# Performance work log

Measured on AMD Instinct MI355X. Metric: run time of the kernel, lower is better.

## Reference

```python
import jax, jax.numpy as jnp
import numpy as np

D = 768
CTX = 64


def ln(x, g, b, eps=1e-5):
    m = x.mean(-1, keepdims=True)
    v = jnp.mean((x - m) ** 2, -1, keepdims=True)
    return (x - m) / jnp.sqrt(v + eps) * g + b


def setup_inputs() -> dict:
    key = jax.random.key(0)
    ks = jax.random.split(key, 16)
    B, N = 16, 1024
    w = lambda k, shape: jax.random.normal(k, shape, dtype=jnp.float32) * 0.02
    return {
        'comps': jax.random.normal(ks[0], (8, B, N, D), jnp.float32),
        'geometric_context': jax.random.normal(ks[1], (B, N, D), jnp.float32),
        'question_features': jax.random.normal(ks[2], (B, D), jnp.float32),
        'spatial_mask': jax.random.randint(ks[3], (B,), 0, 2) > 0,
        'gp_w1': w(ks[4], (D, D // 2)), 'gp_b1': jnp.zeros((D // 2,)),
        'gp_g1': jnp.ones((D // 2,)), 'gp_be1': jnp.zeros((D // 2,)),
        'gp_w2': w(ks[5], (D // 2, CTX)), 'gp_b2': jnp.zeros((CTX,)),
        'swp_w1': w(ks[6], (CTX + D, 256)), 'swp_b1': jnp.zeros((256,)),
        'swp_g1': jnp.ones((256,)), 'swp_be1': jnp.zeros((256,)),
        'swp_w2': w(ks[7], (256, 128)), 'swp_b2': jnp.zeros((128,)),
        'swp_g2': jnp.ones((128,)), 'swp_be2': jnp.zeros((128,)),
        'swp_w3': w(ks[8], (128, 8)), 'swp_b3': jnp.zeros((8,)),
        'sw1': w(ks[9], (4, D + CTX, D)), 'sb1': jnp.zeros((4, D)),
        'sg1': jnp.ones((4, D)), 'sbe1': jnp.zeros((4, D)),
        'sw2': w(ks[10], (4, D, D)), 'sb2': jnp.zeros((4, D)),
        'sg2': jnp.ones((4, D)), 'sbe2': jnp.zeros((4, D)),
        'rw1': w(ks[11], (4, D + CTX, D)), 'rb1': jnp.zeros((4, D)),
        'rg1': jnp.ones((4, D)), 'rbe1': jnp.zeros((4, D)),
        'rw2': w(ks[12], (4, D, D)), 'rb2': jnp.zeros((4, D)),
    }


def reference(comps, geometric_context, question_features, spatial_mask,
              gp_w1, gp_b1, gp_g1, gp_be1, gp_w2, gp_b2,
              swp_w1, swp_b1, swp_g1, swp_be1, swp_w2, swp_b2, swp_g2, swp_be2, swp_w3, swp_b3,
              sw1, sb1, sg1, sbe1, sw2, sb2, sg2, sbe2,
              rw1, rb1, rg1, rbe1, rw2, rb2):
    B, N = geometric_context.shape[:2]
    # geometric_processor on mean-pooled context -> [B, 64]
    gcc = jax.nn.relu(ln(geometric_context.mean(1) @ gp_w1 + gp_b1, gp_g1, gp_be1)) @ gp_w2 + gp_b2
    # spatial_weight_predictor -> softmax weights [B, 8]
    wi = jnp.concatenate([gcc, question_features], -1)
    h = jax.nn.gelu(ln(wi @ swp_w1 + swp_b1, swp_g1, swp_be1), approximate=False)
    h = jax.nn.gelu(ln(h @ swp_w2 + swp_b2, swp_g2, swp_be2), approximate=False)
    aw = jax.nn.softmax(h @ swp_w3 + swp_b3, -1)
    # expanded context; non-spatial samples use 0.1-scaled context for spatial-set comps
    ctx = jnp.broadcast_to(gcc[:, None, :], (B, N, CTX))
    ctx_s = ctx * jnp.where(spatial_mask, 1.0, 0.1)[:, None, None]
    # strong enhancers (GELU, second LN): P_unique(0), V_unique(1), PV(3), PT(5) - all spatial-set
    xs = jnp.concatenate([comps[jnp.array([0, 1, 3, 5])],
                          jnp.broadcast_to(ctx_s, (4, B, N, CTX))], -1)
    h = jax.nn.gelu(ln(jnp.einsum('kbnd,kdf->kbnf', xs, sw1) + sb1[:, None, None, :],
                       sg1[:, None, None, :], sbe1[:, None, None, :]), approximate=False)
    ys = ln(jnp.einsum('kbnd,kdf->kbnf', h, sw2) + sb2[:, None, None, :],
            sg2[:, None, None, :], sbe2[:, None, None, :])
    # ReLU enhancers (moderate/minimal share structure): TV(4, scaled ctx), T_unique(2), redundant(6), higher(7)
    ctx_r = jnp.stack([ctx_s, ctx, ctx, ctx], 0)
    xr = jnp.concatenate([comps[jnp.array([4, 2, 6, 7])], ctx_r], -1)
    h = jax.nn.relu(ln(jnp.einsum('kbnd,kdf->kbnf', xr, rw1) + rb1[:, None, None, :],
                       rg1[:, None, None, :], rbe1[:, None, None, :]))
    yr = jnp.einsum('kbnd,kdf->kbnf', h, rw2) + rb2[:, None, None, :]
    # non-spatial components pass through when spatial_mask is False
    m = spatial_mask[:, None, None]
    out = jnp.stack([
        ys[0],                              # P_unique
        ys[1],                              # V_unique
        jnp.where(m, yr[1], comps[2]),      # T_unique
        ys[2],                              # PV_synergy
        yr[0],                              # TV_synergy
        ys[3],                              # PT_synergy
        jnp.where(m, yr[2], comps[6]),      # redundant
        jnp.where(m, yr[3], comps[7]),      # higher_synergy
    ], 0)
    return out, aw
```

## Files before the change

kernel.cpp:

```cpp
#include <hip/hip_runtime.h>
#include <math.h>

#define MT 16384
#define DD 768
#define AW_OFF ((size_t)8 * MT * DD)

typedef __attribute__((ext_vector_type(8))) short short8;
typedef __attribute__((ext_vector_type(4))) float f32x4;
typedef __attribute__((ext_vector_type(4))) float fv4;
typedef __attribute__((ext_vector_type(4))) unsigned int u32x4;

#define OFF_W1T 0ULL
#define OFF_W2T 10223616ULL
#define OFF_Z1  19660800ULL
#define OFF_Z2  220987392ULL
#define OFF_P1  321675264ULL
#define OFF_P2  324820992ULL
#define OFF_ST1 326393856ULL
#define OFF_ST2 327442432ULL
#define OFF_GP  327966720ULL
#define OFF_GM  328359936ULL
#define OFF_CXS 328409088ULL
#define OFF_CXU 328411136ULL
#define OFF_A1  335544320ULL

static __device__ __forceinline__ unsigned short f2bf(float f) {
  unsigned u = __float_as_uint(f);
  u += 0x7fffu + ((u >> 16) & 1u);
  return (unsigned short)(u >> 16);
}
static __device__ __forceinline__ float bf2f(unsigned short h) {
  return __uint_as_float(((unsigned)h) << 16);
}
static __device__ __forceinline__ unsigned pk2(float lo, float hi) {
  return (unsigned)f2bf(lo) | ((unsigned)f2bf(hi) << 16);
}
static __device__ __forceinline__ float gelu_t(float y) {
  float y2 = y * y;
  float c = fmaf(y2, 0.0713548163f, 1.59576912161f);
  float e = __expf(-y * c);
  return y / (1.0f + e);
}
static __device__ __forceinline__ void gload_lds16(const void* g, void* l) {
  __builtin_amdgcn_global_load_lds(
      (const __attribute__((address_space(1))) void*)g,
      (__attribute__((address_space(3))) void*)l, 16, 0, 0);
}

__global__ void transpose_cvt(const float* sw1, const float* rw1,
                              const float* sw2, const float* rw2,
                              unsigned short* w1T, unsigned short* w2T) {
  __shared__ float t[32][33];
  const int z = blockIdx.z;
  int R; const float* sp; unsigned short* dp;
  if (z < 8) {
    R = 832;
    sp = ((z < 4) ? sw1 : rw1) + (size_t)(z & 3) * 832 * DD;
    dp = w1T + (size_t)z * DD * 832;
  } else {
    R = 768;
    int zz = z - 8;
    sp = ((zz < 4) ? sw2 : rw2) + (size_t)(zz & 3) * DD * DD;
    dp = w2T + (size_t)zz * DD * DD;
  }
  const int r0 = blockIdx.x * 32, c0 = blockIdx.y * 32;
  if (r0 >= R) return;
  const int tx = threadIdx.x & 31, ty = threadIdx.x >> 5;
#pragma unroll
  for (int i = 0; i < 4; i++) {
    int r = ty + i * 8;
    t[r][tx] = sp[(size_t)(r0 + r) * DD + c0 + tx];
  }
  __syncthreads();
#pragma unroll
  for (int i = 0; i < 4; i++) {
    int cc = ty + i * 8;
    dp[(size_t)(c0 + cc) * R + r0 + tx] = f2bf(t[tx][cc]);
  }
}

__global__ void colmean1(const float* __restrict__ geo, float* __restrict__ gp) {
  const int b = blockIdx.z, yc = blockIdx.y;
  const int col = blockIdx.x * 256 + threadIdx.x;
  const float* p = geo + (size_t)b * 1024 * DD + (size_t)yc * 128 * DD + col;
  float s = 0.f;
  for (int n = 0; n < 128; ++n) s += p[(size_t)n * DD];
  gp[((size_t)b * 8 + yc) * DD + col] = s;
}
__global__ void colmean2(const float* __restrict__ gp, float* __restrict__ gm) {
  const int b = blockIdx.y;
  const int col = blockIdx.x * 256 + threadIdx.x;
  float s = 0.f;
#pragma unroll
  for (int i = 0; i < 8; ++i) s += gp[((size_t)b * 8 + i) * DD + col];
  gm[(size_t)b * DD + col] = s * (1.0f / 1024.0f);
}

static __device__ float2 blk_sum2(float a, float b, float* red) {
  const int tid = threadIdx.x;
  __syncthreads();
  red[tid] = a; red[512 + tid] = b;
  if (tid < 128) { red[384 + tid] = 0.f; red[512 + 384 + tid] = 0.f; }
  __syncthreads();
  for (int s = 256; s > 0; s >>= 1) {
    if (tid < s) { red[tid] += red[tid + s]; red[512 + tid] += red[512 + tid + s]; }
    __syncthreads();
  }
  return make_float2(red[0], red[512]);
}

__global__ void small_mlp(
    const float* __restrict__ gc_mean, const float* __restrict__ qf,
    const int* __restrict__ mask,
    const float* __restrict__ gp_w1, const float* __restrict__ gp_b1,
    const float* __restrict__ gp_g1, const float* __restrict__ gp_be1,
    const float* __restrict__ gp_w2, const float* __restrict__ gp_b2,
    const float* __restrict__ swp_w1, const float* __restrict__ swp_b1,
    const float* __restrict__ swp_g1, const float* __restrict__ swp_be1,
    const float* __restrict__ swp_w2, const float* __restrict__ swp_b2,
    const float* __restrict__ swp_g2, const float* __restrict__ swp_be2,
    const float* __restrict__ swp_w3, const float* __restrict__ swp_b3,
    unsigned short* __restrict__ ctxs, unsigned short* __restrict__ ctxu,
    float* __restrict__ aw)
{
  __shared__ float gm[768];
  __shared__ float buf[832];
  __shared__ float tmp[384];
  __shared__ float red[1024];
  const int b = blockIdx.x, tid = threadIdx.x;

  for (int i = tid; i < 768; i += 384) gm[i] = gc_mean[b * 768 + i];
  __syncthreads();

  float z = gp_b1[tid];
  for (int k = 0; k < 768; k++) z += gm[k] * gp_w1[k * 384 + tid];
  float2 s = blk_sum2(z, z * z, red);
  {
    float mean = s.x * (1.f / 384.f);
    float rinv = rsqrtf(s.y * (1.f / 384.f) - mean * mean + 1e-5f);
    float y = (z - mean) * rinv * gp_g1[tid] + gp_be1[tid];
    tmp[tid] = fmaxf(y, 0.f);
  }
  __syncthreads();

  if (tid < 64) {
    float g = gp_b2[tid];
    for (int k = 0; k < 384; k++) g += tmp[k] * gp_w2[k * 64 + tid];
    float sc = (mask[b] != 0) ? 1.0f : 0.1f;
    ctxs[b * 64 + tid] = f2bf(g * sc);
    ctxu[b * 64 + tid] = f2bf(g);
    buf[tid] = g;
  }
  for (int i = tid; i < 768; i += 384) buf[64 + i] = qf[b * 768 + i];
  __syncthreads();

  float z1 = 0.f;
  if (tid < 256) {
    z1 = swp_b1[tid];
    for (int k = 0; k < 832; k++) z1 += buf[k] * swp_w1[k * 256 + tid];
  }
  s = blk_sum2(z1, z1 * z1, red);
  {
    float mean = s.x * (1.f / 256.f);
    float rinv = rsqrtf(s.y * (1.f / 256.f) - mean * mean + 1e-5f);
    if (tid < 256) {
      float y = (z1 - mean) * rinv * swp_g1[tid] + swp_be1[tid];
      tmp[tid] = 0.5f * y * (1.f + erff(y * 0.7071067811865476f));
    }
  }
  __syncthreads();

  float z2 = 0.f;
  if (tid < 128) {
    z2 = swp_b2[tid];
    for (int k = 0; k < 256; k++) z2 += tmp[k] * swp_w2[k * 128 + tid];
  }
  s = blk_sum2(z2, z2 * z2, red);
  {
    float mean = s.x * (1.f / 128.f);
    float rinv = rsqrtf(s.y * (1.f / 128.f) - mean * mean + 1e-5f);
    if (tid < 128) {
      float y = (z2 - mean) * rinv * swp_g2[tid] + swp_be2[tid];
      tmp[tid] = 0.5f * y * (1.f + erff(y * 0.7071067811865476f));
    }
  }
  __syncthreads();

  if (tid < 8) {
    float z3 = swp_b3[tid];
    for (int k = 0; k < 128; k++) z3 += tmp[k] * swp_w3[k * 8 + tid];
    buf[tid] = z3;
  }
  __syncthreads();
  if (tid < 8) {
    float mx = buf[0];
    for (int k = 1; k < 8; k++) mx = fmaxf(mx, buf[k]);
    float ssum = 0.f;
    for (int k = 0; k < 8; k++) ssum += expf(buf[k] - mx);
    aw[b * 8 + tid] = expf(buf[tid] - mx) / ssum;
  }
}

__global__ void stats_k(const float2* __restrict__ part, float2* __restrict__ st,
                        int nr) {
  int i = blockIdx.x * 256 + threadIdx.x;
  if (i >= nr) return;
  float2 p0 = part[i], p1 = part[nr + i], p2 = part[2 * nr + i];
  float s1 = p0.x + p1.x + p2.x, s2 = p0.y + p1.y + p2.y;
  float mean = s1 * (1.f / 768.f);
  float var = s2 * (1.f / 768.f) - mean * mean;
  float rinv = rsqrtf(var + 1e-5f);
  st[i] = make_float2(rinv, -mean * rinv);
}

__global__ __launch_bounds__(512, 4)
void gemm1_k(const float* __restrict__ comps,
             const unsigned short* __restrict__ cxs,
             const unsigned short* __restrict__ cxu,
             const unsigned short* __restrict__ w1T,
             const float* __restrict__ sb1, const float* __restrict__ rb1,
             unsigned short* __restrict__ z1,
             float2* __restrict__ part1,
             const int* __restrict__ mask)
{
  __shared__ __align__(16) unsigned short As[2][4096];
  __shared__ __align__(16) unsigned short Bs[2][8192];
  __shared__ float pscr[4][128][2];
  constexpr int NT = 26;

  const int id = blockIdx.x;
  const int x = id & 7, j = id >> 3;
  const int br_nt = j >> 4;
  const int mt = ((j & 15) << 3) | x;
  const int nt = br_nt % 3;
  const int br = br_nt / 3;
  const int m0 = mt * 128, n0 = nt * 256;
  const int b = m0 >> 10;
  if (br >= 5 && mask[b] == 0) return;

  const int ci = (0x76245310u >> (br * 4)) & 15;
  const float* afp = comps + (size_t)ci * MT * DD + (size_t)m0 * DD;
  const unsigned short* ctxp = ((br <= 4) ? cxs : cxu) + b * 64;
  const unsigned short* wT = w1T + (size_t)br * DD * 832 + (size_t)n0 * 832;

  const int tid = threadIdx.x;
  const int w = tid >> 6, lane = tid & 63, llo = lane & 15, lhi = lane >> 4;
  const int wm = w & 1, wn = w >> 1;

  const int arow = tid >> 2, ap = tid & 3;
  const int aslot = (arow * 32 + ((ap ^ ((arow >> 1) & 3)) << 3));
  const float* asrc = afp + (size_t)arow * DD + ap * 8;
  const unsigned short* csrc = ctxp + ap * 8;

  const int q = lane & 3, rrB = w * 16 + (lane >> 2);
  const int swqB = q ^ ((rrB >> 1) & 3);
  const unsigned short* bsrc0 = wT + (size_t)rrB * 832 + swqB * 8;
  const unsigned short* bsrc1 = wT + (size_t)(128 + rrB) * 832 + swqB * 8;

  f32x4 acc[4][4];
#pragma unroll
  for (int mf = 0; mf < 4; ++mf)
#pragma unroll
    for (int nf = 0; nf < 4; ++nf) acc[mf][nf] = (f32x4)0.0f;

  struct St { u32x4 q0, q1; };

  auto issueB = [&](int kt, int s) {
    gload_lds16(bsrc0 + (size_t)kt * 32, &Bs[s][w * 512]);
    gload_lds16(bsrc1 + (size_t)kt * 32, &Bs[s][4096 + w * 512]);
  };
  auto loadA = [&](int kt) -> St {
    St s;
    if (kt < 24) {
      const u32x4* p = (const u32x4*)(asrc + kt * 32);
      s.q0 = p[0]; s.q1 = p[1];
    } else {
      s.q0 = *(const u32x4*)(csrc + (kt - 24) * 32);
      s.q1 = s.q0;
    }
    return s;
  };
  auto commitA = [&](const St& s, int kt, int sl) {
    u32x4 v;
    if (kt < 24) {
      v[0] = pk2(__uint_as_float(s.q0[0]), __uint_as_float(s.q0[1]));
      v[1] = pk2(__uint_as_float(s.q0[2]), __uint_as_float(s.q0[3]));
      v[2] = pk2(__uint_as_float(s.q1[0]), __uint_as_float(s.q1[1]));
      v[3] = pk2(__uint_as_float(s.q1[2]), __uint_as_float(s.q1[3]));
    } else {
      v = s.q0;
    }
    *(u32x4*)&As[sl][aslot] = v;
  };

  const int aswz = (lhi ^ ((llo >> 1) & 3)) << 3;
  const int arow0 = (wm * 64 + llo) * 32 + aswz;
  const int brow0 = (wn * 64 + llo) * 32 + aswz;
  auto compute = [&](int sl) {
    short8 afr[4];
#pragma unroll
    for (int mf = 0; mf < 4; ++mf)
      afr[mf] = *(const short8*)&As[sl][arow0 + mf * 512];
#pragma unroll
    for (int nf = 0; nf < 4; ++nf) {
      short8 bfr = *(const short8*)&Bs[sl][brow0 + nf * 512];
#pragma unroll
      for (int mf = 0; mf < 4; ++mf)
        acc[mf][nf] = __builtin_amdgcn_mfma_f32_16x16x32_bf16(afr[mf], bfr, acc[mf][nf], 0, 0, 0);
    }
  };

  issueB(0, 0);
  {
    St s0 = loadA(0);
    commitA(s0, 0, 0);
  }
  asm volatile("s_waitcnt lgkmcnt(0)" ::: "memory");
  __builtin_amdgcn_sched_barrier(0);
  __builtin_amdgcn_s_barrier();

#pragma unroll 1
  for (int t = 0; t < NT; ++t) {
    const int cur = t & 1, nxt = cur ^ 1;
    const bool more = (t + 1 < NT);
    St sn;
    if (more) {
      issueB(t + 1, nxt);
      sn = loadA(t + 1);
    }
    __builtin_amdgcn_sched_barrier(0);
    compute(cur);
    __builtin_amdgcn_sched_barrier(0);
    if (more) commitA(sn, t + 1, nxt);
    asm volatile("s_waitcnt lgkmcnt(0)" ::: "memory");
    __builtin_amdgcn_sched_barrier(0);
    __builtin_amdgcn_s_barrier();
  }

  const float* bias = ((br < 4) ? sb1 : rb1) + (br & 3) * DD;
  unsigned short* zo = z1 + (size_t)br * MT * DD + (size_t)m0 * DD;
  const int n0w = n0 + wn * 64;
  float bia[4];
#pragma unroll
  for (int nf = 0; nf < 4; ++nf) bia[nf] = bias[n0w + nf * 16 + llo];
#pragma unroll
  for (int mf = 0; mf < 4; ++mf) {
#pragma unroll
    for (int r = 0; r < 4; ++r) {
      float zz[4]; float s1v = 0.f, s2v = 0.f;
#pragma unroll
      for (int nf = 0; nf < 4; ++nf) {
        float zv = acc[mf][nf][r] + bia[nf];
        zz[nf] = zv; s1v += zv; s2v += zv * zv;
      }
      const int rloc = wm * 64 + mf * 16 + lhi * 4 + r;
      const size_t rowoff = (size_t)rloc * DD;
#pragma unroll
      for (int nf = 0; nf < 4; ++nf) {
        float zon = __shfl_xor(zz[nf], 1);
        if ((llo & 1) == 0)
          *(unsigned*)&zo[rowoff + n0w + nf * 16 + llo] = pk2(zz[nf], zon);
      }
#pragma unroll
      for (int d = 1; d < 16; d <<= 1) {
        s1v += __shfl_xor(s1v, d); s2v += __shfl_xor(s2v, d);
      }
      if (llo == 0) { pscr[wn][rloc][0] = s1v; pscr[wn][rloc][1] = s2v; }
    }
  }
  __syncthreads();
  if (tid < 128) {
    float a = 0.f, c = 0.f;
#pragma unroll
    for (int qq = 0; qq < 4; ++qq) { a += pscr[qq][tid][0]; c += pscr[qq][tid][1]; }
    part1[(size_t)nt * (8 * MT) + (size_t)br * MT + m0 + tid] = make_float2(a, c);
  }
}

__global__ void act1_k(const unsigned short* __restrict__ z1,
                       const float2* __restrict__ st1,
                       const float* __restrict__ sg1, const float* __restrict__ sbe1,
                       const float* __restrict__ rg1, const float* __restrict__ rbe1,
                       const int* __restrict__ mask,
                       unsigned short* __restrict__ a1)
{
  const int tid = threadIdx.x;
  const int rowg = blockIdx.x * 8 + (tid >> 5);
  const int l = tid & 31;
  const int br = rowg >> 14;
  const int r = rowg & 16383;
  const int b = r >> 10;
  if (br >= 5 && mask[b] == 0) return;
  const bool isg = (br < 4);
  const float* g  = (isg ? sg1  + br * DD : rg1  + (br - 4) * DD);
  const float* be = (isg ? sbe1 + br * DD : rbe1 + (br - 4) * DD);
  const float2 stv = st1[rowg];
  const unsigned short* zp = z1 + (size_t)rowg * DD;
  unsigned short* op = a1 + (size_t)rowg * DD;
#pragma unroll
  for (int c = 0; c < 3; ++c) {
    const int col = l * 8 + c * 256;
    u32x4 zv = *(const u32x4*)(zp + col);
    fv4 ga = *(const fv4*)(g + col), gb = *(const fv4*)(g + col + 4);
    fv4 ba = *(const fv4*)(be + col), bb = *(const fv4*)(be + col + 4);
    float y[8];
#pragma unroll
    for (int wd = 0; wd < 2; ++wd) {
      y[2*wd]   = fmaf(fmaf(bf2f((unsigned short)(zv[wd] & 0xffffu)), stv.x, stv.y), ga[2*wd], ba[2*wd]);
      y[2*wd+1] = fmaf(fmaf(bf2f((unsigned short)(zv[wd] >> 16)), stv.x, stv.y), ga[2*wd+1], ba[2*wd+1]);
      y[4+2*wd]   = fmaf(fmaf(bf2f((unsigned short)(zv[wd+2] & 0xffffu)), stv.x, stv.y), gb[2*wd], bb[2*wd]);
      y[4+2*wd+1] = fmaf(fmaf(bf2f((unsigned short)(zv[wd+2] >> 16)), stv.x, stv.y), gb[2*wd+1], bb[2*wd+1]);
    }
    u32x4 ov;
#pragma unroll
    for (int wd = 0; wd < 4; ++wd) {
      float y0 = y[2*wd], y1 = y[2*wd+1];
      if (isg) { y0 = gelu_t(y0); y1 = gelu_t(y1); }
      else     { y0 = fmaxf(y0, 0.f); y1 = fmaxf(y1, 0.f); }
      ov[wd] = pk2(y0, y1);
    }
    *(u32x4*)(op + col) = ov;
  }
}

__global__ __launch_bounds__(512, 4)
void gemm2_k(const float* __restrict__ comps,
             const unsigned short* __restrict__ a1,
             const unsigned short* __restrict__ w2T,
             const float* __restrict__ sb2, const float* __restrict__ rb2,
             unsigned short* __restrict__ z2,
             float2* __restrict__ part2,
             float* __restrict__ outp,
             const int* __restrict__ mask)
{
  __shared__ __align__(16) unsigned short As[3][4096];
  __shared__ __align__(16) unsigned short Bs[3][8192];
  __shared__ float pscr[4][128][2];
  constexpr int NT = 24;

  const int id = blockIdx.x;
  const int x = id & 7, j = id >> 3;
  const int br_nt = j >> 4;
  const int mt = ((j & 15) << 3) | x;
  const int nt = br_nt % 3;
  const int br = br_nt / 3;
  const int m0 = mt * 128, n0 = nt * 256;
  const int b = m0 >> 10;
  const int ci = (0x76245310u >> (br * 4)) & 15;
  const int tid = threadIdx.x;

  if (br >= 5 && mask[b] == 0) {
    const float* cs = comps + (size_t)ci * MT * DD + (size_t)m0 * DD + n0;
    float* cd = outp + (size_t)ci * MT * DD + (size_t)m0 * DD + n0;
#pragma unroll 1
    for (int k = 0; k < 16; ++k) {
      int idx = tid + k * 512;
      int r2 = idx >> 6, c4 = (idx & 63) * 4;
      *(fv4*)(cd + (size_t)r2 * DD + c4) = *(const fv4*)(cs + (size_t)r2 * DD + c4);
    }
    return;
  }

  const unsigned short* az = a1 + (size_t)br * MT * DD + (size_t)m0 * DD;
  const unsigned short* wT = w2T + (size_t)br * DD * DD + (size_t)n0 * DD;

  const int w = tid >> 6, lane = tid & 63, llo = lane & 15, lhi = lane >> 4;
  const int wm = w & 1, wn = w >> 1;
  const int q = lane & 3, rrB = w * 16 + (lane >> 2);
  const int swqB = q ^ ((rrB >> 1) & 3);

  const unsigned short* asrcD = az + (size_t)rrB * DD + swqB * 8;
  const unsigned short* bsrc0 = wT + (size_t)rrB * DD + swqB * 8;
  const unsigned short* bsrc1 = wT + (size_t)(128 + rrB) * DD + swqB * 8;

  f32x4 acc[4][4];
#pragma unroll
  for (int mf = 0; mf < 4; ++mf)
#pragma unroll
    for (int nf = 0; nf < 4; ++nf) acc[mf][nf] = (f32x4)0.0f;

  auto issueT = [&](int kt, int s) {
    gload_lds16(asrcD + (size_t)kt * 32, &As[s][w * 512]);
    gload_lds16(bsrc0 + (size_t)kt * 32, &Bs[s][w * 512]);
    gload_lds16(bsrc1 + (size_t)kt * 32, &Bs[s][4096 + w * 512]);
  };

  const int aswz = (lhi ^ ((llo >> 1) & 3)) << 3;
  const int arow0 = (wm * 64 + llo) * 32 + aswz;
  const int brow0 = (wn * 64 + llo) * 32 + aswz;
  auto compute = [&](int sl) {
    short8 afr[4];
#pragma unroll
    for (int mf = 0; mf < 4; ++mf)
      afr[mf] = *(const short8*)&As[sl][arow0 + mf * 512];
#pragma unroll
    for (int nf = 0; nf < 4; ++nf) {
      short8 bfr = *(const short8*)&Bs[sl][brow0 + nf * 512];
#pragma unroll
      for (int mf = 0; mf < 4; ++mf)
        acc[mf][nf] = __builtin_amdgcn_mfma_f32_16x16x32_bf16(afr[mf], bfr, acc[mf][nf], 0, 0, 0);
    }
  };

  issueT(0, 0);
  issueT(1, 1);
  asm volatile("s_waitcnt vmcnt(3)" ::: "memory");
  __builtin_amdgcn_sched_barrier(0);
  __builtin_amdgcn_s_barrier();

  int sl = 0;
#pragma unroll 1
  for (int t = 0; t < NT; ++t) {
    int sl2 = sl + 2; if (sl2 >= 3) sl2 -= 3;
    const bool more = (t + 2 < NT);
    if (more) issueT(t + 2, sl2);
    __builtin_amdgcn_sched_barrier(0);
    compute(sl);
    if (more) asm volatile("s_waitcnt vmcnt(3)" ::: "memory");
    else      asm volatile("s_waitcnt vmcnt(0)" ::: "memory");
    asm volatile("s_waitcnt lgkmcnt(0)" ::: "memory");
    __builtin_amdgcn_sched_barrier(0);
    __builtin_amdgcn_s_barrier();
    ++sl; if (sl == 3) sl = 0;
  }

  const int n0w = n0 + wn * 64;
  const float* bias = ((br < 4) ? sb2 : rb2) + (br & 3) * DD;
  float bia[4];
#pragma unroll
  for (int nf = 0; nf < 4; ++nf) bia[nf] = bias[n0w + nf * 16 + llo];

  if (br < 4) {
    unsigned short* zo = z2 + (size_t)br * MT * DD + (size_t)m0 * DD;
#pragma unroll
    for (int mf = 0; mf < 4; ++mf) {
#pragma unroll
      for (int r = 0; r < 4; ++r) {
        float zz[4]; float s1v = 0.f, s2v = 0.f;
#pragma unroll
        for (int nf = 0; nf < 4; ++nf) {
          float zv = acc[mf][nf][r] + bia[nf];
          zz[nf] = zv; s1v += zv; s2v += zv * zv;
        }
        const int rloc = wm * 64 + mf * 16 + lhi * 4 + r;
        const size_t rowoff = (size_t)rloc * DD;
#pragma unroll
        for (int nf = 0; nf < 4; ++nf) {
          float zon = __shfl_xor(zz[nf], 1);
          if ((llo & 1) == 0)
            *(unsigned*)&zo[rowoff + n0w + nf * 16 + llo] = pk2(zz[nf], zon);
        }
#pragma unroll
        for (int d = 1; d < 16; d <<= 1) {
          s1v += __shfl_xor(s1v, d); s2v += __shfl_xor(s2v, d);
        }
        if (llo == 0) { pscr[wn][rloc][0] = s1v; pscr[wn][rloc][1] = s2v; }
      }
    }
    __syncthreads();
    if (tid < 128) {
      float a = 0.f, c = 0.f;
#pragma unroll
      for (int qq = 0; qq < 4; ++qq) { a += pscr[qq][tid][0]; c += pscr[qq][tid][1]; }
      part2[(size_t)nt * (4 * MT) + (size_t)br * MT + m0 + tid] = make_float2(a, c);
    }
  } else {
    float* fo = outp + (size_t)ci * MT * DD + (size_t)m0 * DD;
#pragma unroll
    for (int mf = 0; mf < 4; ++mf) {
#pragma unroll
      for (int r = 0; r < 4; ++r) {
        const int rloc = wm * 64 + mf * 16 + lhi * 4 + r;
        const size_t rowoff = (size_t)rloc * DD;
#pragma unroll
        for (int nf = 0; nf < 4; ++nf)
          fo[rowoff + n0w + nf * 16 + llo] = acc[mf][nf][r] + bia[nf];
      }
    }
  }
}

__global__ void finish_s(const unsigned short* __restrict__ z2,
                         const float2* __restrict__ st2,
                         const float* __restrict__ sg2,
                         const float* __restrict__ sbe2,
                         float* __restrict__ outp)
{
  const int tid = threadIdx.x;
  const int rowg = blockIdx.x * 8 + (tid >> 5);
  const int l = tid & 31;
  const int br = rowg >> 14;
  const int r = rowg & 16383;
  const int ci = (0x5310u >> (br * 4)) & 15;
  const unsigned short* zp = z2 + (size_t)rowg * DD;
  float* op = outp + (size_t)ci * MT * DD + (size_t)r * DD;
  const float2 stv = st2[rowg];
  const float* g = sg2 + br * DD;
  const float* be = sbe2 + br * DD;
#pragma unroll
  for (int c = 0; c < 3; ++c) {
    const int col = l * 8 + c * 256;
    u32x4 zv = *(const u32x4*)(zp + col);
    fv4 ga = *(const fv4*)(g + col), gb = *(const fv4*)(g + col + 4);
    fv4 ba = *(const fv4*)(be + col), bb = *(const fv4*)(be + col + 4);
    fv4 o0, o1;
#pragma unroll
    for (int wd = 0; wd < 2; ++wd) {
      o0[2 * wd]     = fmaf(fmaf(bf2f((unsigned short)(zv[wd] & 0xffffu)), stv.x, stv.y), ga[2 * wd], ba[2 * wd]);
      o0[2 * wd + 1] = fmaf(fmaf(bf2f((unsigned short)(zv[wd] >> 16)), stv.x, stv.y), ga[2 * wd + 1], ba[2 * wd + 1]);
      o1[2 * wd]     = fmaf(fmaf(bf2f((unsigned short)(zv[wd + 2] & 0xffffu)), stv.x, stv.y), gb[2 * wd], bb[2 * wd]);
      o1[2 * wd + 1] = fmaf(fmaf(bf2f((unsigned short)(zv[wd + 2] >> 16)), stv.x, stv.y), gb[2 * wd + 1], bb[2 * wd + 1]);
    }
    *(fv4*)(op + col) = o0;
    *(fv4*)(op + col + 4) = o1;
  }
}

extern "C" void kernel_launch(void* const* d_in, const int* in_sizes, int n_in,
                              void* d_out, int out_size, void* d_ws, size_t ws_size,
                              hipStream_t stream)
{
  (void)in_sizes; (void)n_in; (void)out_size; (void)ws_size;
  const float* comps  = (const float*)d_in[0];
  const float* geo    = (const float*)d_in[1];
  const float* qf     = (const float*)d_in[2];
  const int*   mask   = (const int*)d_in[3];
  const float* gp_w1  = (const float*)d_in[4];
  const float* gp_b1  = (const float*)d_in[5];
  const float* gp_g1  = (const float*)d_in[6];
  const float* gp_be1 = (const float*)d_in[7];
  const float* gp_w2  = (const float*)d_in[8];
  const float* gp_b2  = (const float*)d_in[9];
  const float* swp_w1 = (const float*)d_in[10];
  const float* swp_b1 = (const float*)d_in[11];
  const float* swp_g1 = (const float*)d_in[12];
  const float* swp_be1= (const float*)d_in[13];
  const float* swp_w2 = (const float*)d_in[14];
  const float* swp_b2 = (const float*)d_in[15];
  const float* swp_g2 = (const float*)d_in[16];
  const float* swp_be2= (const float*)d_in[17];
  const float* swp_w3 = (const float*)d_in[18];
  const float* swp_b3 = (const float*)d_in[19];
  const float* sw1 = (const float*)d_in[20];
  const float* sb1 = (const float*)d_in[21];
  const float* sg1 = (const float*)d_in[22];
  const float* sbe1= (const float*)d_in[23];
  const float* sw2 = (const float*)d_in[24];
  const float* sb2 = (const float*)d_in[25];
  const float* sg2 = (const float*)d_in[26];
  const float* sbe2= (const float*)d_in[27];
  const float* rw1 = (const float*)d_in[28];
  const float* rb1 = (const float*)d_in[29];
  const float* rg1 = (const float*)d_in[30];
  const float* rbe1= (const float*)d_in[31];
  const float* rw2 = (const float*)d_in[32];
  const float* rb2 = (const float*)d_in[33];
  float* out = (float*)d_out;

  char* ws = (char*)d_ws;
  unsigned short* w1T = (unsigned short*)(ws + OFF_W1T);
  unsigned short* w2T = (unsigned short*)(ws + OFF_W2T);
  unsigned short* z1  = (unsigned short*)(ws + OFF_Z1);
  unsigned short* z2  = (unsigned short*)(ws + OFF_Z2);
  float2* part1 = (float2*)(ws + OFF_P1);
  float2* part2 = (float2*)(ws + OFF_P2);
  float2* st1   = (float2*)(ws + OFF_ST1);
  float2* st2   = (float2*)(ws + OFF_ST2);
  float* gpart  = (float*)(ws + OFF_GP);
  float* gmean  = (float*)(ws + OFF_GM);
  unsigned short* cxs = (unsigned short*)(ws + OFF_CXS);
  unsigned short* cxu = (unsigned short*)(ws + OFF_CXU);
  unsigned short* a1  = (unsigned short*)(ws + OFF_A1);

  transpose_cvt<<<dim3(26, 24, 16), 256, 0, stream>>>(sw1, rw1, sw2, rw2, w1T, w2T);
  colmean1<<<dim3(3, 8, 16), 256, 0, stream>>>(geo, gpart);
  colmean2<<<dim3(3, 16), 256, 0, stream>>>(gpart, gmean);
  small_mlp<<<16, 384, 0, stream>>>(gmean, qf, mask,
      gp_w1, gp_b1, gp_g1, gp_be1, gp_w2, gp_b2,
      swp_w1, swp_b1, swp_g1, swp_be1, swp_w2, swp_b2, swp_g2, swp_be2,
      swp_w3, swp_b3, cxs, cxu, out + AW_OFF);

  gemm1_k<<<3072, 512, 0, stream>>>(comps, cxs, cxu, w1T, sb1, rb1, z1, part1, mask);
  stats_k<<<512, 256, 0, stream>>>(part1, st1, 8 * MT);
  act1_k<<<16384, 256, 0, stream>>>(z1, st1, sg1, sbe1, rg1, rbe1, mask, a1);
  gemm2_k<<<3072, 512, 0, stream>>>(comps, a1, w2T, sb2, rb2, z2, part2, out, mask);
  stats_k<<<256, 256, 0, stream>>>(part2, st2, 4 * MT);
  finish_s<<<8192, 256, 0, stream>>>(z2, st2, sg2, sbe2, out);
}
```

Baseline: 774.7 us.

## Fold context columns into per-batch bias and retile GEMMs to 128x128

The context part of the first-layer concat is constant per batch, so its product with the last 64 weight rows is precomputed in fp32 by a new ctxbias kernel into a per-batch, per-branch bias. gemm1 then only iterates over K=768. Both GEMMs move from 512-thread 128x256 tiles to 256-thread 128x128 tiles, with twice as many blocks and a 3-stage LDS ring, and gemm1 software-pipelines two A stages ahead. stats_k now reduces six N-partials instead of three. This removes the extra K iterations and the bf16 rounding of the context, but smaller tiles reload the A operand more often.

Result: slower. 865.4 us (+11.7%).

```diff
diff --git a/kernel.cpp b/kernel.cpp
--- a/kernel.cpp
+++ b/kernel.cpp
@@ -14,14 +14,14 @@
 #define OFF_W2T 10223616ULL
 #define OFF_Z1  19660800ULL
 #define OFF_Z2  220987392ULL
-#define OFF_P1  321675264ULL
-#define OFF_P2  324820992ULL
-#define OFF_ST1 326393856ULL
-#define OFF_ST2 327442432ULL
-#define OFF_GP  327966720ULL
-#define OFF_GM  328359936ULL
-#define OFF_CXS 328409088ULL
-#define OFF_CXU 328411136ULL
+#define OFF_P1  321650688ULL
+#define OFF_P2  327942144ULL
+#define OFF_ST1 331087872ULL
+#define OFF_ST2 332136448ULL
+#define OFF_GP  332660736ULL
+#define OFF_GM  333053952ULL
+#define OFF_CXF 333103104ULL
+#define OFF_B1X 333111296ULL
 #define OFF_A1  335544320ULL
 
 static __device__ __forceinline__ unsigned short f2bf(float f) {
@@ -120,7 +120,7 @@
     const float* __restrict__ swp_w2, const float* __restrict__ swp_b2,
     const float* __restrict__ swp_g2, const float* __restrict__ swp_be2,
     const float* __restrict__ swp_w3, const float* __restrict__ swp_b3,
-    unsigned short* __restrict__ ctxs, unsigned short* __restrict__ ctxu,
+    float* __restrict__ cxfs, float* __restrict__ cxfu,
     float* __restrict__ aw)
 {
   __shared__ float gm[768];
@@ -147,8 +147,8 @@
     float g = gp_b2[tid];
     for (int k = 0; k < 384; k++) g += tmp[k] * gp_w2[k * 64 + tid];
     float sc = (mask[b] != 0) ? 1.0f : 0.1f;
-    ctxs[b * 64 + tid] = f2bf(g * sc);
-    ctxu[b * 64 + tid] = f2bf(g);
+    cxfs[b * 64 + tid] = g * sc;
+    cxfu[b * 64 + tid] = g;
     buf[tid] = g;
   }
   for (int i = tid; i < 768; i += 384) buf[64 + i] = qf[b * 768 + i];
@@ -201,61 +201,89 @@
   }
 }
 
+__global__ void ctxbias_k(const float* __restrict__ cxfs,
+                          const float* __restrict__ cxfu,
+                          const float* __restrict__ sw1, const float* __restrict__ rw1,
+                          const float* __restrict__ sb1, const float* __restrict__ rb1,
+                          float* __restrict__ b1x)
+{
+  const int br = blockIdx.x, b = blockIdx.y, tid = threadIdx.x;
+  __shared__ float cf[64];
+  if (tid < 64) cf[tid] = ((br <= 4) ? cxfs : cxfu)[b * 64 + tid];
+  __syncthreads();
+  const float* W = ((br < 4) ? sw1 + (size_t)br * 832 * DD
+                             : rw1 + (size_t)(br - 4) * 832 * DD) + (size_t)768 * DD;
+  const float* bb = (br < 4) ? sb1 + br * DD : rb1 + (br - 4) * DD;
+#pragma unroll
+  for (int jj = 0; jj < 3; ++jj) {
+    const int f = tid + jj * 256;
+    float s = bb[f];
+    for (int k = 0; k < 64; ++k) s += cf[k] * W[(size_t)k * DD + f];
+    b1x[((size_t)br * 16 + b) * DD + f] = s;
+  }
+}
+
 __global__ void stats_k(const float2* __restrict__ part, float2* __restrict__ st,
                         int nr) {
   int i = blockIdx.x * 256 + threadIdx.x;
   if (i >= nr) return;
-  float2 p0 = part[i], p1 = part[nr + i], p2 = part[2 * nr + i];
-  float s1 = p0.x + p1.x + p2.x, s2 = p0.y + p1.y + p2.y;
+  float s1 = 0.f, s2 = 0.f;
+#pragma unroll
+  for (int s = 0; s < 6; ++s) {
+    float2 p = part[(size_t)s * nr + i];
+    s1 += p.x; s2 += p.y;
+  }
   float mean = s1 * (1.f / 768.f);
   float var = s2 * (1.f / 768.f) - mean * mean;
   float rinv = rsqrtf(var + 1e-5f);
   st[i] = make_float2(rinv, -mean * rinv);
 }
 
-__global__ __launch_bounds__(512, 4)
+__global__ __launch_bounds__(256, 3)
 void gemm1_k(const float* __restrict__ comps,
-             const unsigned short* __restrict__ cxs,
-             const unsigned short* __restrict__ cxu,
              const unsigned short* __restrict__ w1T,
-             const float* __restrict__ sb1, const float* __restrict__ rb1,
+             const float* __restrict__ b1x,
              unsigned short* __restrict__ z1,
              float2* __restrict__ part1,
              const int* __restrict__ mask)
 {
-  __shared__ __align__(16) unsigned short As[2][4096];
-  __shared__ __align__(16) unsigned short Bs[2][8192];
-  __shared__ float pscr[4][128][2];
-  constexpr int NT = 26;
+  __shared__ __align__(16) unsigned short As[3][4096];
+  __shared__ __align__(16) unsigned short Bs[3][4096];
+  __shared__ float pscr[2][128][2];
+  constexpr int NT = 24;
 
   const int id = blockIdx.x;
   const int x = id & 7, j = id >> 3;
-  const int br_nt = j >> 4;
-  const int mt = ((j & 15) << 3) | x;
-  const int nt = br_nt % 3;
-  const int br = br_nt / 3;
-  const int m0 = mt * 128, n0 = nt * 256;
+  const int br = j / 96;
+  const int r96 = j - br * 96;
+  const int mg = r96 / 6;
+  const int nt = r96 - mg * 6;
+  const int mt = mg * 8 + x;
+  const int m0 = mt * 128, n0 = nt * 128;
   const int b = m0 >> 10;
   if (br >= 5 && mask[b] == 0) return;
 
   const int ci = (0x76245310u >> (br * 4)) & 15;
   const float* afp = comps + (size_t)ci * MT * DD + (size_t)m0 * DD;
-  const unsigned short* ctxp = ((br <= 4) ? cxs : cxu) + b * 64;
-  const unsigned short* wT = w1T + (size_t)br * DD * 832 + (size_t)n0 * 832;
+  const unsigned short* wT = w1T + (size_t)br * DD * 832;
+  const float* bias = b1x + ((size_t)br * 16 + b) * DD;
+  unsigned short* zo = z1 + (size_t)br * MT * DD + (size_t)m0 * DD;
 
   const int tid = threadIdx.x;
   const int w = tid >> 6, lane = tid & 63, llo = lane & 15, lhi = lane >> 4;
   const int wm = w & 1, wn = w >> 1;
 
-  const int arow = tid >> 2, ap = tid & 3;
-  const int aslot = (arow * 32 + ((ap ^ ((arow >> 1) & 3)) << 3));
-  const float* asrc = afp + (size_t)arow * DD + ap * 8;
-  const unsigned short* csrc = ctxp + ap * 8;
-
-  const int q = lane & 3, rrB = w * 16 + (lane >> 2);
-  const int swqB = q ^ ((rrB >> 1) & 3);
-  const unsigned short* bsrc0 = wT + (size_t)rrB * 832 + swqB * 8;
-  const unsigned short* bsrc1 = wT + (size_t)(128 + rrB) * 832 + swqB * 8;
+  const int swB = (((lane & 3) ^ ((lane >> 3) & 3)) << 3);
+  const unsigned short* bsrc0 =
+      wT + (size_t)(n0 + (w * 2 + 0) * 16 + (lane >> 2)) * 832 + swB;
+  const unsigned short* bsrc1 =
+      wT + (size_t)(n0 + (w * 2 + 1) * 16 + (lane >> 2)) * 832 + swB;
+
+  const int arow = tid >> 1, h = tid & 1;
+  const float* asrc = afp + (size_t)arow * DD + h * 16;
+  const int swA = (arow >> 1) & 3;
+  const int soff0 = arow * 32 + (((2 * h) ^ swA) << 3);
+  const int soff1 = arow * 32 + (((2 * h + 1) ^ swA) << 3);
 
   f32x4 acc[4][4];
 #pragma unroll
@@ -263,34 +291,26 @@
 #pragma unroll
     for (int nf = 0; nf < 4; ++nf) acc[mf][nf] = (f32x4)0.0f;
 
-  struct St { u32x4 q0, q1; };
+  struct St { fv4 a, b2, c, d; };
 
   auto issueB = [&](int kt, int s) {
-    gload_lds16(bsrc0 + (size_t)kt * 32, &Bs[s][w * 512]);
-    gload_lds16(bsrc1 + (size_t)kt * 32, &Bs[s][4096 + w * 512]);
+    gload_lds16(bsrc0 + (size_t)kt * 32, &Bs[s][(w * 2 + 0) * 512]);
+    gload_lds16(bsrc1 + (size_t)kt * 32, &Bs[s][(w * 2 + 1) * 512]);
   };
   auto loadA = [&](int kt) -> St {
     St s;
-    if (kt < 24) {
-      const u32x4* p = (const u32x4*)(asrc + kt * 32);
-      s.q0 = p[0]; s.q1 = p[1];
-    } else {
-      s.q0 = *(const u32x4*)(csrc + (kt - 24) * 32);
-      s.q1 = s.q0;
-    }
+    const fv4* p = (const fv4*)(asrc + kt * 32);
+    s.a = p[0]; s.b2 = p[1]; s.c = p[2]; s.d = p[3];
     return s;
   };
-  auto commitA = [&](const St& s, int kt, int sl) {
-    u32x4 v;
-    if (kt < 24) {
-      v[0] = pk2(__uint_as_float(s.q0[0]), __uint_as_float(s.q0[1]));
-      v[1] = pk2(__uint_as_float(s.q0[2]), __uint_as_float(s.q0[3]));
-      v[2] = pk2(__uint_as_float(s.q1[0]), __uint_as_float(s.q1[1]));
-      v[3] = pk2(__uint_as_float(s.q1[2]), __uint_as_float(s.q1[3]));
-    } else {
-      v = s.q0;
-    }
-    *(u32x4*)&As[sl][aslot] = v;
+  auto commitA = [&](const St& s, int sl) {
+    u32x4 w0, w1;
+    w0[0] = pk2(s.a[0], s.a[1]);  w0[1] = pk2(s.a[2], s.a[3]);
+    w0[2] = pk2(s.b2[0], s.b2[1]); w0[3] = pk2(s.b2[2], s.b2[3]);
+    w1[0] = pk2(s.c[0], s.c[1]);  w1[1] = pk2(s.c[2], s.c[3]);
+    w1[2] = pk2(s.d[0], s.d[1]);  w1[3] = pk2(s.d[2], s.d[3]);
+    *(u32x4*)&As[sl][soff0] = w0;
+    *(u32x4*)&As[sl][soff1] = w1;
   };
 
   const int aswz = (lhi ^ ((llo >> 1) & 3)) << 3;
@@ -311,34 +331,38 @@
   };
 
   issueB(0, 0);
-  {
-    St s0 = loadA(0);
-    commitA(s0, 0, 0);
-  }
+  St sA = loadA(0);
+  issueB(1, 1);
+  St sB = loadA(1);
+  commitA(sA, 0);
   asm volatile("s_waitcnt lgkmcnt(0)" ::: "memory");
   __builtin_amdgcn_sched_barrier(0);
   __builtin_amdgcn_s_barrier();
 
+  int sc = 0;
 #pragma unroll 1
-  for (int t = 0; t < NT; ++t) {
-    const int cur = t & 1, nxt = cur ^ 1;
-    const bool more = (t + 1 < NT);
-    St sn;
-    if (more) {
-      issueB(t + 1, nxt);
-      sn = loadA(t + 1);
-    }
+  for (int t = 0; t < NT; t += 2) {
+    int s1 = sc + 1; if (s1 == 3) s1 = 0;
+    int s2 = s1 + 1; if (s2 == 3) s2 = 0;
+    if (t + 2 < NT) { issueB(t + 2, s2); sA = loadA(t + 2); }
     __builtin_amdgcn_sched_barrier(0);
-    compute(cur);
+    compute(sc);
     __builtin_amdgcn_sched_barrier(0);
-    if (more) commitA(sn, t + 1, nxt);
+    if (t + 1 < NT) commitA(sB, s1);
     asm volatile("s_waitcnt lgkmcnt(0)" ::: "memory");
     __builtin_amdgcn_sched_barrier(0);
     __builtin_amdgcn_s_barrier();
-  }
-
-  const float* bias = ((br < 4) ? sb1 : rb1) + (br & 3) * DD;
-  unsigned short* zo = z1 + (size_t)br * MT * DD + (size_t)m0 * DD;
+    if (t + 3 < NT) { issueB(t + 3, sc); sB = loadA(t + 3); }
+    __builtin_amdgcn_sched_barrier(0);
+    compute(s1);
+    __builtin_amdgcn_sched_barrier(0);
+    if (t + 2 < NT) commitA(sA, s2);
+    asm volatile("s_waitcnt lgkmcnt(0)" ::: "memory");
+    __builtin_amdgcn_sched_barrier(0);
+    __builtin_amdgcn_s_barrier();
+    sc = s2;
+  }
+
   const int n0w = n0 + wn * 64;
   float bia[4];
 #pragma unroll
@@ -370,9 +394,8 @@
   }
   __syncthreads();
   if (tid < 128) {
-    float a = 0.f, c = 0.f;
-#pragma unroll
-    for (int qq = 0; qq < 4; ++qq) { a += pscr[qq][tid][0]; c += pscr[qq][tid][1]; }
+    float a = pscr[0][tid][0] + pscr[1][tid][0];
+    float c = pscr[0][tid][1] + pscr[1][tid][1];
     part1[(size_t)nt * (8 * MT) + (size_t)br * MT + m0 + tid] = make_float2(a, c);
   }
 }
@@ -423,7 +446,7 @@
   }
 }
 
-__global__ __launch_bounds__(512, 4)
+__global__ __launch_bounds__(256, 3)
 void gemm2_k(const float* __restrict__ comps,
              const unsigned short* __restrict__ a1,
              const unsigned short* __restrict__ w2T,
@@ -434,17 +457,18 @@
              const int* __restrict__ mask)
 {
   __shared__ __align__(16) unsigned short As[3][4096];
-  __shared__ __align__(16) unsigned short Bs[3][8192];
-  __shared__ float pscr[4][128][2];
+  __shared__ __align__(16) unsigned short Bs[3][4096];
+  __shared__ float pscr[2][128][2];
   constexpr int NT = 24;
 
   const int id = blockIdx.x;
   const int x = id & 7, j = id >> 3;
-  const int br_nt = j >> 4;
-  const int mt = ((j & 15) << 3) | x;
-  const int nt = br_nt % 3;
-  const int br = br_nt / 3;
-  const int m0 = mt * 128, n0 = nt * 256;
+  const int br = j / 96;
+  const int r96 = j - br * 96;
+  const int mg = r96 / 6;
+  const int nt = r96 - mg * 6;
+  const int mt = mg * 8 + x;
+  const int m0 = mt * 128, n0 = nt * 128;
   const int b = m0 >> 10;
   const int ci = (0x76245310u >> (br * 4)) & 15;
   const int tid = threadIdx.x;
@@ -454,24 +478,24 @@
     float* cd = outp + (size_t)ci * MT * DD + (size_t)m0 * DD + n0;
 #pragma unroll 1
     for (int k = 0; k < 16; ++k) {
-      int idx = tid + k * 512;
-      int r2 = idx >> 6, c4 = (idx & 63) * 4;
+      int idx = tid + k * 256;
+      int r2 = idx >> 5, c4 = (idx & 31) * 4;
       *(fv4*)(cd + (size_t)r2 * DD + c4) = *(const fv4*)(cs + (size_t)r2 * DD + c4);
     }
     return;
   }
 
   const unsigned short* az = a1 + (size_t)br * MT * DD + (size_t)m0 * DD;
-  const unsigned short* wT = w2T + (size_t)br * DD * DD + (size_t)n0 * DD;
+  const unsigned short* wT = w2T + (size_t)br * DD * DD;
 
   const int w = tid >> 6, lane = tid & 63, llo = lane & 15, lhi = lane >> 4;
   const int wm = w & 1, wn = w >> 1;
-  const int q = lane & 3, rrB = w * 16 + (lane >> 2);
-  const int swqB = q ^ ((rrB >> 1) & 3);
-
-  const unsigned short* asrcD = az + (size_t)rrB * DD + swqB * 8;
-  const unsigned short* bsrc0 = wT + (size_t)rrB * DD + swqB * 8;
-  const unsigned short* bsrc1 = wT + (size_t)(128 + rrB) * DD + swqB * 8;
+
+  const int swB = (((lane & 3) ^ ((lane >> 3) & 3)) << 3);
+  const unsigned short* asrc0 = az + (size_t)((w * 2 + 0) * 16 + (lane >> 2)) * DD + swB;
+  const unsigned short* asrc1 = az + (size_t)((w * 2 + 1) * 16 + (lane >> 2)) * DD + swB;
+  const unsigned short* bsrc0 = wT + (size_t)(n0 + (w * 2 + 0) * 16 + (lane >> 2)) * DD + swB;
+  const unsigned short* bsrc1 = wT + (size_t)(n0 + (w * 2 + 1) * 16 + (lane >> 2)) * DD + swB;
 
   f32x4 acc[4][4];
 #pragma unroll
@@ -480,9 +504,10 @@
     for (int nf = 0; nf < 4; ++nf) acc[mf][nf] = (f32x4)0.0f;
 
   auto issueT = [&](int kt, int s) {
-    gload_lds16(asrcD + (size_t)kt * 32, &As[s][w * 512]);
-    gload_lds16(bsrc0 + (size_t)kt * 32, &Bs[s][w * 512]);
-    gload_lds16(bsrc1 + (size_t)kt * 32, &Bs[s][4096 + w * 512]);
+    gload_lds16(asrc0 + (size_t)kt * 32, &As[s][(w * 2 + 0) * 512]);
+    gload_lds16(asrc1 + (size_t)kt * 32, &As[s][(w * 2 + 1) * 512]);
+    gload_lds16(bsrc0 + (size_t)kt * 32, &Bs[s][(w * 2 + 0) * 512]);
+    gload_lds16(bsrc1 + (size_t)kt * 32, &Bs[s][(w * 2 + 1) * 512]);
   };
 
   const int aswz = (lhi ^ ((llo >> 1) & 3)) << 3;
@@ -504,24 +529,23 @@
 
   issueT(0, 0);
   issueT(1, 1);
-  asm volatile("s_waitcnt vmcnt(3)" ::: "memory");
+  asm volatile("s_waitcnt vmcnt(4)" ::: "memory");
   __builtin_amdgcn_sched_barrier(0);
   __builtin_amdgcn_s_barrier();
 
-  int sl = 0;
+  int sc = 0;
 #pragma unroll 1
   for (int t = 0; t < NT; ++t) {
-    int sl2 = sl + 2; if (sl2 >= 3) sl2 -= 3;
+    int s2 = sc + 2; if (s2 >= 3) s2 -= 3;
     const bool more = (t + 2 < NT);
-    if (more) issueT(t + 2, sl2);
+    if (more) issueT(t + 2, s2);
     __builtin_amdgcn_sched_barrier(0);
-    compute(sl);
-    if (more) asm volatile("s_waitcnt vmcnt(3)" ::: "memory");
+    compute(sc);
+    if (more) asm volatile("s_waitcnt vmcnt(4)" ::: "memory");
     else      asm volatile("s_waitcnt vmcnt(0)" ::: "memory");
-    asm volatile("s_waitcnt lgkmcnt(0)" ::: "memory");
     __builtin_amdgcn_sched_barrier(0);
     __builtin_amdgcn_s_barrier();
-    ++sl; if (sl == 3) sl = 0;
+    ++sc; if (sc == 3) sc = 0;
   }
 
   const int n0w = n0 + wn * 64;
@@ -559,9 +583,8 @@
     }
     __syncthreads();
     if (tid < 128) {
-      float a = 0.f, c = 0.f;
-#pragma unroll
-      for (int qq = 0; qq < 4; ++qq) { a += pscr[qq][tid][0]; c += pscr[qq][tid][1]; }
+      float a = pscr[0][tid][0] + pscr[1][tid][0];
+      float c = pscr[0][tid][1] + pscr[1][tid][1];
       part2[(size_t)nt * (4 * MT) + (size_t)br * MT + m0 + tid] = make_float2(a, c);
     }
   } else {
@@ -668,9 +691,10 @@
   float2* st2   = (float2*)(ws + OFF_ST2);
   float* gpart  = (float*)(ws + OFF_GP);
   float* gmean  = (float*)(ws + OFF_GM);
-  unsigned short* cxs = (unsigned short*)(ws + OFF_CXS);
-  unsigned short* cxu = (unsigned short*)(ws + OFF_CXU);
-  unsigned short* a1  = (unsigned short*)(ws + OFF_A1);
+  float* cxfs   = (float*)(ws + OFF_CXF);
+  float* cxfu   = (float*)(ws + OFF_CXF + 4096);
+  float* b1x    = (float*)(ws + OFF_B1X);
+  unsigned short* a1 = (unsigned short*)(ws + OFF_A1);
 
   transpose_cvt<<<dim3(26, 24, 16), 256, 0, stream>>>(sw1, rw1, sw2, rw2, w1T, w2T);
   colmean1<<<dim3(3, 8, 16), 256, 0, stream>>>(geo, gpart);
@@ -678,12 +702,13 @@
   small_mlp<<<16, 384, 0, stream>>>(gmean, qf, mask,
       gp_w1, gp_b1, gp_g1, gp_be1, gp_w2, gp_b2,
       swp_w1, swp_b1, swp_g1, swp_be1, swp_w2, swp_b2, swp_g2, swp_be2,
-      swp_w3, swp_b3, cxs, cxu, out + AW_OFF);
-
-  gemm1_k<<<3072, 512, 0, stream>>>(comps, cxs, cxu, w1T, sb1, rb1, z1, part1, mask);
+      swp_w3, swp_b3, cxfs, cxfu, out + AW_OFF);
+  ctxbias_k<<<dim3(8, 16), 256, 0, stream>>>(cxfs, cxfu, sw1, rw1, sb1, rb1, b1x);
+
+  gemm1_k<<<6144, 256, 0, stream>>>(comps, w1T, b1x, z1, part1, mask);
   stats_k<<<512, 256, 0, stream>>>(part1, st1, 8 * MT);
   act1_k<<<16384, 256, 0, stream>>>(z1, st1, sg1, sbe1, rg1, rbe1, mask, a1);
-  gemm2_k<<<3072, 512, 0, stream>>>(comps, a1, w2T, sb2, rb2, z2, part2, out, mask);
+  gemm2_k<<<6144, 256, 0, stream>>>(comps, a1, w2T, sb2, rb2, z2, part2, out, mask);
   stats_k<<<256, 256, 0, stream>>>(part2, st2, 4 * MT);
   finish_s<<<8192, 256, 0, stream>>>(z2, st2, sg2, sbe2, out);
 }
```
